# Optimization experiments

Hardware: AMD Instinct MI355X
Metric: run time of the kernel (lower is better)

## Reference

```python
import jax, jax.numpy as jnp
import numpy as np

B, G, C = 16384, 7, 30  # batch, 7x7 grid, 2*5 box params + 20 classes


def setup_inputs() -> dict:
    key = jax.random.key(0)
    k1, k2 = jax.random.split(key)
    pred = jax.random.uniform(k1, (B, G, G, C), dtype=jnp.float32)
    labels = jax.random.uniform(k2, (B, G, G, C), dtype=jnp.float32)
    # channel 0 of labels is the object-presence indicator (==1 where a gt box exists)
    labels = labels.at[..., 0].set((labels[..., 0] > 0.7).astype(jnp.float32))
    return {"pred": pred, "labels": labels}


def _corners(box):
    # box channels: [conf, x, y, w, h]
    x, y, w, h = box[..., 1], box[..., 2], box[..., 3], box[..., 4]
    return x - 0.5 * w, x + 0.5 * w, y - 0.5 * h, y + 0.5 * h  # left,right,top,bottom


def _iou(b1, b2):
    l1, r1, t1, bt1 = _corners(b1)
    l2, r2, t2, bt2 = _corners(b2)
    in_h = jnp.minimum(bt1, bt2) - jnp.maximum(t1, t2)
    in_w = jnp.minimum(r1, r2) - jnp.maximum(l1, l2)
    inter = jnp.where((in_h < 0) | (in_w < 0), 0.0, in_h * in_w)
    area1 = (bt1 - t1) * (r1 - l1)
    area2 = (bt2 - t2) * (r2 - l2)
    return inter / (area1 + area2 - inter)


def reference(pred, labels):
    mask = labels[..., 0]                     # [B,7,7] object indicator (0/1)
    box1 = pred[..., 0:5]
    box2 = pred[..., 5:10]
    gt = labels[..., 0:5]
    iou1 = _iou(box1, gt)
    iou2 = _iou(box2, gt)
    best = iou1 >= iou2                       # responsible box per cell
    sel = jnp.where(best[..., None], box1, box2)
    iou_max = jnp.where(best, iou1, iou2)
    iou_min = jnp.where(best, iou2, iou1)
    center = 5.0 * ((sel[..., 1] - gt[..., 1]) ** 2 + (sel[..., 2] - gt[..., 2]) ** 2)
    wh = 5.0 * ((jnp.sqrt(sel[..., 3]) - jnp.sqrt(gt[..., 3])) ** 2
                + (jnp.sqrt(sel[..., 4]) - jnp.sqrt(gt[..., 4])) ** 2)
    cls = jnp.sum((pred[..., 10:] - labels[..., 10:]) ** 2, axis=-1)

    def msum(x):
        return jnp.sum(x * mask)

    # [center, wh, obj_conf, noobj_conf, classification]
    return jnp.stack([msum(center), msum(wh), msum(iou_max), msum(iou_min), msum(cls)])
```

## Files before the change

kernel.cpp:

```cpp
#include <hip/hip_runtime.h>

#define NCH 30
#define CPB 256
#define TPB 256

__device__ __forceinline__ float iou_f(float x1, float y1, float w1, float h1,
                                       float x2, float y2, float w2, float h2) {
    float l1 = x1 - 0.5f * w1, r1 = x1 + 0.5f * w1;
    float t1 = y1 - 0.5f * h1, b1 = y1 + 0.5f * h1;
    float l2 = x2 - 0.5f * w2, r2 = x2 + 0.5f * w2;
    float t2 = y2 - 0.5f * h2, b2 = y2 + 0.5f * h2;
    float in_h = fminf(b1, b2) - fmaxf(t1, t2);
    float in_w = fminf(r1, r2) - fmaxf(l1, l2);
    float inter = (in_h < 0.f || in_w < 0.f) ? 0.f : in_h * in_w;
    float a1 = (b1 - t1) * (r1 - l1);
    float a2 = (b2 - t2) * (r2 - l2);
    return inter / (a1 + a2 - inter);
}

__global__ __launch_bounds__(TPB) void yolo_partial(const float* __restrict__ pred,
                                                    const float* __restrict__ lab,
                                                    float* __restrict__ partial) {
    __shared__ float s_p[CPB * NCH];
    __shared__ float s_l[CPB * NCH];
    __shared__ float red[5][TPB / 64];

    const int tid = threadIdx.x;
    const size_t base_vec = (size_t)blockIdx.x * (CPB * NCH / 4);

    const float4* gp = (const float4*)pred + base_vec;
    const float4* gl = (const float4*)lab + base_vec;
    float4* sp = (float4*)s_p;
    float4* sl = (float4*)s_l;
#pragma unroll
    for (int i = 0; i < CPB * NCH / 4; i += TPB) {
        sp[i + tid] = gp[i + tid];
        sl[i + tid] = gl[i + tid];
    }
    __syncthreads();

    const float* cp = s_p + tid * NCH;
    const float* cl = s_l + tid * NCH;
    float mask = cl[0];
    float gx = cl[1], gy = cl[2], gw = cl[3], gh = cl[4];

    float i1 = iou_f(cp[1], cp[2], cp[3], cp[4], gx, gy, gw, gh);
    float i2 = iou_f(cp[6], cp[7], cp[8], cp[9], gx, gy, gw, gh);
    bool best = (i1 >= i2);
    float sx = best ? cp[1] : cp[6];
    float sy = best ? cp[2] : cp[7];
    float sw = best ? cp[3] : cp[8];
    float sh = best ? cp[4] : cp[9];
    float imax = best ? i1 : i2;
    float imin = best ? i2 : i1;

    float center = 5.f * ((sx - gx) * (sx - gx) + (sy - gy) * (sy - gy));
    float dw = sqrtf(sw) - sqrtf(gw);
    float dh = sqrtf(sh) - sqrtf(gh);
    float wh = 5.f * (dw * dw + dh * dh);

    float cls = 0.f;
#pragma unroll
    for (int c = 10; c < 30; ++c) {
        float d = cp[c] - cl[c];
        cls += d * d;
    }

    float v0 = center * mask;
    float v1 = wh * mask;
    float v2 = imax * mask;
    float v3 = imin * mask;
    float v4 = cls * mask;

#pragma unroll
    for (int off = 32; off > 0; off >>= 1) {
        v0 += __shfl_down(v0, off);
        v1 += __shfl_down(v1, off);
        v2 += __shfl_down(v2, off);
        v3 += __shfl_down(v3, off);
        v4 += __shfl_down(v4, off);
    }

    const int wave = tid >> 6;
    const int lane = tid & 63;
    if (lane == 0) {
        red[0][wave] = v0;
        red[1][wave] = v1;
        red[2][wave] = v2;
        red[3][wave] = v3;
        red[4][wave] = v4;
    }
    __syncthreads();

    if (tid < 5) {
        float s = 0.f;
#pragma unroll
        for (int w = 0; w < TPB / 64; ++w) s += red[tid][w];
        partial[(size_t)blockIdx.x * 5 + tid] = s;
    }
}

__global__ __launch_bounds__(256) void final_reduce(const float* __restrict__ partial,
                                                    float* __restrict__ out,
                                                    int n_blocks) {
    __shared__ float red[5][4];
    const int tid = threadIdx.x;
    float v0 = 0.f, v1 = 0.f, v2 = 0.f, v3 = 0.f, v4 = 0.f;
    for (int b = tid; b < n_blocks; b += 256) {
        const float* p = partial + (size_t)b * 5;
        v0 += p[0]; v1 += p[1]; v2 += p[2]; v3 += p[3]; v4 += p[4];
    }
#pragma unroll
    for (int off = 32; off > 0; off >>= 1) {
        v0 += __shfl_down(v0, off);
        v1 += __shfl_down(v1, off);
        v2 += __shfl_down(v2, off);
        v3 += __shfl_down(v3, off);
        v4 += __shfl_down(v4, off);
    }
    const int wave = tid >> 6;
    const int lane = tid & 63;
    if (lane == 0) {
        red[0][wave] = v0;
        red[1][wave] = v1;
        red[2][wave] = v2;
        red[3][wave] = v3;
        red[4][wave] = v4;
    }
    __syncthreads();
    if (tid < 5) {
        float s = 0.f;
#pragma unroll
        for (int w = 0; w < 4; ++w) s += red[tid][w];
        out[tid] = s;
    }
}

extern "C" void kernel_launch(void* const* d_in, const int* in_sizes, int n_in,
                              void* d_out, int out_size, void* d_ws, size_t ws_size,
                              hipStream_t stream) {
    const float* pred = (const float*)d_in[0];
    const float* lab  = (const float*)d_in[1];
    float* out = (float*)d_out;
    float* partial = (float*)d_ws;

    const int n_cells = in_sizes[0] / NCH;
    const int grid = n_cells / CPB;

    hipLaunchKernelGGL(yolo_partial, dim3(grid), dim3(TPB), 0, stream,
                       pred, lab, partial);
    hipLaunchKernelGGL(final_reduce, dim3(1), dim3(256), 0, stream,
                       partial, out, grid);
}
```

Before: 208.5 us.

## Load directly from global memory and skip prediction reads for empty cells

Drops the LDS staging of full prediction and label tiles. Each thread now reads its own cell straight from global memory with float2 loads, checks the object mask first, and only loads predictions and runs the IoU and loss math when the mask is nonzero. This aims to cut prediction traffic for the majority of empty cells and remove the large shared-memory footprint that limited occupancy. The trade-off is strided, less coalesced per-thread loads, and it treats masked cells as exactly zero even when their values would be non-finite.

```diff
diff --git a/kernel.cpp b/kernel.cpp
--- a/kernel.cpp
+++ b/kernel.cpp
@@ -1,7 +1,6 @@
 #include <hip/hip_runtime.h>
 
 #define NCH 30
-#define CPB 256
 #define TPB 256
 
 __device__ __forceinline__ float iou_f(float x1, float y1, float w1, float h1,
@@ -20,57 +19,63 @@
 
 __global__ __launch_bounds__(TPB) void yolo_partial(const float* __restrict__ pred,
                                                     const float* __restrict__ lab,
-                                                    float* __restrict__ partial) {
-    __shared__ float s_p[CPB * NCH];
-    __shared__ float s_l[CPB * NCH];
+                                                    float* __restrict__ partial,
+                                                    int n_cells) {
     __shared__ float red[5][TPB / 64];
+    const int tid = threadIdx.x;
+    const size_t c = (size_t)blockIdx.x * TPB + tid;
 
-    const int tid = threadIdx.x;
-    const size_t base_vec = (size_t)blockIdx.x * (CPB * NCH / 4);
+    float v0 = 0.f, v1 = 0.f, v2 = 0.f, v3 = 0.f, v4 = 0.f;
 
-    const float4* gp = (const float4*)pred + base_vec;
-    const float4* gl = (const float4*)lab + base_vec;
-    float4* sp = (float4*)s_p;
-    float4* sl = (float4*)s_l;
+    if (c < (size_t)n_cells) {
+        const float* lp = lab + c * NCH;
+        const float2 l01 = *(const float2*)(lp);
+        const float mask = l01.x;
+
+        if (mask != 0.f) {
+            const float* pp = pred + c * NCH;
+            const float2 l23 = *(const float2*)(lp + 2);
+            const float2 l45 = *(const float2*)(lp + 4);
+            const float gx = l01.y, gy = l23.x, gw = l23.y, gh = l45.x;
+
+            const float2 p01 = *(const float2*)(pp);
+            const float2 p23 = *(const float2*)(pp + 2);
+            const float2 p45 = *(const float2*)(pp + 4);
+            const float2 p67 = *(const float2*)(pp + 6);
+            const float2 p89 = *(const float2*)(pp + 8);
+
+            const float i1 = iou_f(p01.y, p23.x, p23.y, p45.x, gx, gy, gw, gh);
+            const float i2 = iou_f(p67.x, p67.y, p89.x, p89.y, gx, gy, gw, gh);
+            const bool best = (i1 >= i2);
+            const float sx = best ? p01.y : p67.x;
+            const float sy = best ? p23.x : p67.y;
+            const float sw = best ? p23.y : p89.x;
+            const float sh = best ? p45.x : p89.y;
+            const float imax = best ? i1 : i2;
+            const float imin = best ? i2 : i1;
+
+            const float center = 5.f * ((sx - gx) * (sx - gx) + (sy - gy) * (sy - gy));
+            const float dw = sqrtf(sw) - sqrtf(gw);
+            const float dh = sqrtf(sh) - sqrtf(gh);
+            const float wh = 5.f * (dw * dw + dh * dh);
+
+            float cls = 0.f;
 #pragma unroll
-    for (int i = 0; i < CPB * NCH / 4; i += TPB) {
-        sp[i + tid] = gp[i + tid];
-        sl[i + tid] = gl[i + tid];
+            for (int k = 0; k < 10; ++k) {
+                const float2 pd = *(const float2*)(pp + 10 + 2 * k);
+                const float2 ld = *(const float2*)(lp + 10 + 2 * k);
+                const float dx = pd.x - ld.x;
+                const float dy = pd.y - ld.y;
+                cls += dx * dx + dy * dy;
+            }
+
+            v0 = center * mask;
+            v1 = wh * mask;
+            v2 = imax * mask;
+            v3 = imin * mask;
+            v4 = cls * mask;
+        }
     }
-    __syncthreads();
-
-    const float* cp = s_p + tid * NCH;
-    const float* cl = s_l + tid * NCH;
-    float mask = cl[0];
-    float gx = cl[1], gy = cl[2], gw = cl[3], gh = cl[4];
-
-    float i1 = iou_f(cp[1], cp[2], cp[3], cp[4], gx, gy, gw, gh);
-    float i2 = iou_f(cp[6], cp[7], cp[8], cp[9], gx, gy, gw, gh);
-    bool best = (i1 >= i2);
-    float sx = best ? cp[1] : cp[6];
-    float sy = best ? cp[2] : cp[7];
-    float sw = best ? cp[3] : cp[8];
-    float sh = best ? cp[4] : cp[9];
-    float imax = best ? i1 : i2;
-    float imin = best ? i2 : i1;
-
-    float center = 5.f * ((sx - gx) * (sx - gx) + (sy - gy) * (sy - gy));
-    float dw = sqrtf(sw) - sqrtf(gw);
-    float dh = sqrtf(sh) - sqrtf(gh);
-    float wh = 5.f * (dw * dw + dh * dh);
-
-    float cls = 0.f;
-#pragma unroll
-    for (int c = 10; c < 30; ++c) {
-        float d = cp[c] - cl[c];
-        cls += d * d;
-    }
-
-    float v0 = center * mask;
-    float v1 = wh * mask;
-    float v2 = imax * mask;
-    float v3 = imin * mask;
-    float v4 = cls * mask;
 
 #pragma unroll
     for (int off = 32; off > 0; off >>= 1) {
@@ -145,10 +150,10 @@
     float* partial = (float*)d_ws;
 
     const int n_cells = in_sizes[0] / NCH;
-    const int grid = n_cells / CPB;
+    const int grid = (n_cells + TPB - 1) / TPB;
 
     hipLaunchKernelGGL(yolo_partial, dim3(grid), dim3(TPB), 0, stream,
-                       pred, lab, partial);
+                       pred, lab, partial, n_cells);
     hipLaunchKernelGGL(final_reduce, dim3(1), dim3(256), 0, stream,
                        partial, out, grid);
 }
```

Result: faster. 203.2 us (-2.6%).
